# Performance work log

Hardware: AMD Instinct MI355X
Metric: run time of the kernel (lower is better)

The kernel has to match this reference:

```python
import jax, jax.numpy as jnp
import numpy as np

BLOCK_SIZE = 256
EMB = 384
HEAD = 64
B = 256
T = 256

def setup_inputs() -> dict:
    key = jax.random.key(0)
    k1, k2, k3, k4 = jax.random.split(key, 4)
    x = jax.random.normal(k1, (B, T, EMB), dtype=jnp.float32)
    # torch Linear(no bias) default init ~ U(-1/sqrt(in), 1/sqrt(in)); use scaled normal
    s = 1.0 / np.sqrt(EMB)
    Wq = jax.random.normal(k2, (EMB, HEAD), dtype=jnp.float32) * s
    Wk = jax.random.normal(k3, (EMB, HEAD), dtype=jnp.float32) * s
    Wv = jax.random.normal(k4, (EMB, HEAD), dtype=jnp.float32) * s
    return {"x": x, "Wq": Wq, "Wk": Wk, "Wv": Wv}

def reference(x, Wq, Wk, Wv):
    Bb, Tt, C = x.shape
    q = jnp.einsum('btc,ch->bth', x, Wq)
    k = jnp.einsum('btc,ch->bth', x, Wk)
    v = jnp.einsum('btc,ch->bth', x, Wv)
    # NOTE: source scales by C**-0.5 where C = embedding dim (384), not head_size
    scores = jnp.einsum('bth,bsh->bts', q, k) * (C ** -0.5)  # [B,T,T]
    causal = jnp.tril(jnp.ones((Tt, Tt), dtype=bool))
    scores = jnp.where(causal, scores, -jnp.inf)
    weights = jax.nn.softmax(scores, axis=-1)
    # dropout is identity in eval mode (reference baseline)
    out = jnp.einsum('bts,bsh->bth', weights, v)
    return out
```

## Files before the change

### kernel.cpp

```cpp
#include <hip/hip_runtime.h>
#include <hip/hip_bf16.h>
#include <cstdint>
#include <cstddef>

#define B_DIM 256
#define T_DIM 256
#define EMB   384
#define HEAD  64

typedef __attribute__((ext_vector_type(8))) short bf16x8;
typedef __attribute__((ext_vector_type(4))) float f32x4;
typedef __attribute__((ext_vector_type(4))) unsigned int u32x4;

__device__ __forceinline__ unsigned short f2bf(float f) {
    union { float f; unsigned int u; } v; v.f = f;
    unsigned int r = v.u + 0x7fffu + ((v.u >> 16) & 1u);
    return (unsigned short)(r >> 16);
}

__device__ __forceinline__ unsigned int pkbf(float a, float b) {
#if __has_builtin(__builtin_amdgcn_cvt_pk_bf16_f32)
    typedef __attribute__((ext_vector_type(2))) __bf16 bf16x2_t;
    bf16x2_t r = __builtin_amdgcn_cvt_pk_bf16_f32(a, b);
    return *(unsigned int*)&r;
#else
    return (unsigned)f2bf(a) | ((unsigned)f2bf(b) << 16);
#endif
}

__global__ void wprep_kernel(const float* __restrict__ Wq, const float* __restrict__ Wk,
                             const float* __restrict__ Wv, unsigned short* __restrict__ Wb) {
    int g = blockIdx.x * blockDim.x + threadIdx.x;
    if (g >= 9216) return;
    int kkstep = g / 1536, rem = g - kkstep * 1536;
    int r = rem >> 3, cs = rem & 7, c = cs ^ (r & 7);
    const float* W = (r < 64) ? Wq : (r < 128) ? Wk : Wv;
    int h = r & 63;
    unsigned short tmp[8];
#pragma unroll
    for (int e = 0; e < 8; ++e) {
        int k = kkstep * 64 + c * 8 + e;
        tmp[e] = f2bf(W[k * HEAD + h]);
    }
    *(u32x4*)(Wb + (size_t)g * 8) = *(u32x4*)tmp;
}

__global__ __launch_bounds__(1024, 1) void fused_kernel(const float* __restrict__ x,
                                                        const unsigned short* __restrict__ Wb,
                                                        float* __restrict__ out) {
    __shared__ union SM {
        struct { unsigned short Xs[2][256][72]; unsigned short Ws[2][12288]; } p1;
        struct { unsigned short qs[256][72]; unsigned short ks[256][72];
                 unsigned short vT[64][264]; unsigned short Ps[16][16][72]; } p2;
    } sm;

    const int tid = threadIdx.x;
    const int w = tid >> 6, lane = tid & 63, qd = lane >> 4, l15 = lane & 15;
    const int wm = w >> 2, wn = w & 3;
    const int b = blockIdx.x;
    const float* xb = x + (size_t)b * T_DIM * EMB;
    const int xrow = tid >> 2, xj = tid & 3;

#define WGLDS(KSTEP, BUF) do { \
    _Pragma("unroll") \
    for (int s = 0; s < 2; ++s) { \
        int idx = s * 1024 + w * 64; \
        if (idx < 1536) { \
            const unsigned short* gp = Wb + (size_t)((KSTEP) * 1536 + idx + lane) * 8; \
            unsigned short* lp = &sm.p1.Ws[BUF][idx * 8]; \
            __builtin_amdgcn_global_load_lds( \
                (const __attribute__((address_space(1))) unsigned int*)gp, \
                (__attribute__((address_space(3))) unsigned int*)lp, 16, 0, 0); \
        } \
    } \
} while (0)

#define XLOAD(KK) do { \
    _Pragma("unroll") \
    for (int i = 0; i < 4; ++i) \
        xr[i] = *(const float4*)(xb + (size_t)xrow * EMB + (KK) * 64 + (4 * xj + i) * 4); \
} while (0)

#define XWRITE(BUF) do { \
    _Pragma("unroll") \
    for (int i = 0; i < 4; ++i) \
        *(uint2*)&sm.p1.Xs[BUF][xrow][4 * (4 * xj + i)] = \
            make_uint2(pkbf(xr[i].x, xr[i].y), pkbf(xr[i].z, xr[i].w)); \
} while (0)

    float4 xr[4];
    WGLDS(0, 0);
    XLOAD(0);
    XWRITE(0);

    f32x4 acc[4][3];
#pragma unroll
    for (int mt = 0; mt < 4; ++mt)
#pragma unroll
        for (int nt = 0; nt < 3; ++nt) acc[mt][nt] = (f32x4){0.f, 0.f, 0.f, 0.f};

#pragma unroll
    for (int kk = 0; kk < 6; ++kk) {
        __syncthreads();
        if (kk < 5) {
            WGLDS(kk + 1, (kk + 1) & 1);
            XLOAD(kk + 1);
        }
#pragma unroll
        for (int kb = 0; kb < 2; ++kb) {
            bf16x8 a[4], bb[3];
#pragma unroll
            for (int mt = 0; mt < 4; ++mt)
                a[mt] = *(const bf16x8*)&sm.p1.Xs[kk & 1][64 * wm + 16 * mt + l15][32 * kb + 8 * qd];
#pragma unroll
            for (int nt = 0; nt < 3; ++nt) {
                int n = 48 * wn + 16 * nt + l15;
                bb[nt] = *(const bf16x8*)&sm.p1.Ws[kk & 1][n * 64 + (((4 * kb + qd) ^ (n & 7)) << 3)];
            }
#pragma unroll
            for (int mt = 0; mt < 4; ++mt)
#pragma unroll
                for (int nt = 0; nt < 3; ++nt)
                    acc[mt][nt] = __builtin_amdgcn_mfma_f32_16x16x32_bf16(a[mt], bb[nt], acc[mt][nt], 0, 0, 0);
        }
        if (kk < 5) XWRITE((kk + 1) & 1);
    }
    __syncthreads();

#pragma unroll
    for (int nt = 0; nt < 3; ++nt) {
        int n = 48 * wn + 16 * nt + l15;
        int arr = n >> 6, hh = n & 63;
        if (arr == 2) {
#pragma unroll
            for (int mt = 0; mt < 4; ++mt) {
                int tok0 = 64 * wm + 16 * mt + 4 * qd;
                *(uint2*)&sm.p2.vT[hh][tok0] = make_uint2(
                    pkbf(acc[mt][nt][0], acc[mt][nt][1]),
                    pkbf(acc[mt][nt][2], acc[mt][nt][3]));
            }
        } else {
#pragma unroll
            for (int mt = 0; mt < 4; ++mt)
#pragma unroll
                for (int reg = 0; reg < 4; ++reg) {
                    int tok = 64 * wm + 16 * mt + 4 * qd + reg;
                    unsigned short val = f2bf(acc[mt][nt][reg]);
                    if (arr == 0) sm.p2.qs[tok][hh] = val;
                    else          sm.p2.ks[tok][hh] = val;
                }
        }
    }
    __syncthreads();

    const int slot = w >> 2, sid = w & 3;
    const int t = (slot < 2) ? (2 * sid + slot) : (15 - 2 * sid - (slot & 1));

    bf16x8 aq[2];
#pragma unroll
    for (int kbi = 0; kbi < 2; ++kbi)
        aq[kbi] = *(const bf16x8*)&sm.p2.qs[16 * t + l15][32 * kbi + 8 * qd];

    f32x4 O[4];
    float l[4];
#pragma unroll
    for (int dn = 0; dn < 4; ++dn) O[dn] = (f32x4){0.f, 0.f, 0.f, 0.f};
#pragma unroll
    for (int reg = 0; reg < 4; ++reg) l[reg] = 0.f;

    const float cExp = 1.4426950408889634f / 19.595917942265423f;

    for (int jc = 0; jc <= (t >> 2); ++jc) {
        const int ntmax = min(3, t - 4 * jc);
        f32x4 S[4];
#pragma unroll
        for (int nt = 0; nt < 4; ++nt) {
            if (nt <= ntmax) {
                bf16x8 b0 = *(const bf16x8*)&sm.p2.ks[64 * jc + 16 * nt + l15][8 * qd];
                bf16x8 b1 = *(const bf16x8*)&sm.p2.ks[64 * jc + 16 * nt + l15][32 + 8 * qd];
                f32x4 s = __builtin_amdgcn_mfma_f32_16x16x32_bf16(aq[0], b0, (f32x4){0.f,0.f,0.f,0.f}, 0, 0, 0);
                s = __builtin_amdgcn_mfma_f32_16x16x32_bf16(aq[1], b1, s, 0, 0, 0);
                S[nt] = s;
            }
        }
#pragma unroll
        for (int nt = 0; nt < 4; ++nt) {
#pragma unroll
            for (int reg = 0; reg < 4; ++reg) {
                float p = 0.0f;
                if (nt <= ntmax) {
                    p = exp2f(S[nt][reg] * cExp);
                    if (4 * jc + nt == t && (l15 > 4 * qd + reg)) p = 0.0f;
                }
                l[reg] += p;
                sm.p2.Ps[w][4 * qd + reg][16 * nt + l15] = f2bf(p);
            }
        }
        bf16x8 ap0 = *(const bf16x8*)&sm.p2.Ps[w][l15][8 * qd];
        bf16x8 ap1 = *(const bf16x8*)&sm.p2.Ps[w][l15][32 + 8 * qd];
#pragma unroll
        for (int dn = 0; dn < 4; ++dn) {
            bf16x8 bv0 = *(const bf16x8*)&sm.p2.vT[16 * dn + l15][64 * jc + 8 * qd];
            bf16x8 bv1 = *(const bf16x8*)&sm.p2.vT[16 * dn + l15][64 * jc + 32 + 8 * qd];
            O[dn] = __builtin_amdgcn_mfma_f32_16x16x32_bf16(ap0, bv0, O[dn], 0, 0, 0);
            O[dn] = __builtin_amdgcn_mfma_f32_16x16x32_bf16(ap1, bv1, O[dn], 0, 0, 0);
        }
    }

#pragma unroll
    for (int reg = 0; reg < 4; ++reg) {
        float s = l[reg];
        s += __shfl_xor(s, 1);
        s += __shfl_xor(s, 2);
        s += __shfl_xor(s, 4);
        s += __shfl_xor(s, 8);
        float inv = 1.0f / s;
        int row = 16 * t + 4 * qd + reg;
        float* dst = out + ((size_t)b * T_DIM + row) * HEAD;
#pragma unroll
        for (int dn = 0; dn < 4; ++dn)
            dst[16 * dn + l15] = O[dn][reg] * inv;
    }
}

extern "C" void kernel_launch(void* const* d_in, const int* in_sizes, int n_in,
                              void* d_out, int out_size, void* d_ws, size_t ws_size,
                              hipStream_t stream) {
    const float* x  = (const float*)d_in[0];
    const float* Wq = (const float*)d_in[1];
    const float* Wk = (const float*)d_in[2];
    const float* Wv = (const float*)d_in[3];
    float* out = (float*)d_out;

    unsigned short* Wb = (unsigned short*)d_ws;

    wprep_kernel<<<36, 256, 0, stream>>>(Wq, Wk, Wv, Wb);
    fused_kernel<<<B_DIM, 1024, 0, stream>>>(x, Wb, out);
}
```

Before: 173.0 us.

## Warp-specialize projection GEMM into producer and consumer waves

The QKV projection phase now splits waves: 4 producer waves issue all global loads of x and W into LDS for the next stage, while 12 consumer waves run the MFMA projection with a 4x4 tile per wave (one of Q/K/V per wave column). This aims to overlap global memory latency with tensor math and drop load work from the compute waves. In exchange it removes a quarter of the waves from MFMA work, so each compute wave does more, and producer waves hold more registers.

```diff
diff --git a/kernel.cpp b/kernel.cpp
--- a/kernel.cpp
+++ b/kernel.cpp
@@ -56,99 +56,111 @@
 
     const int tid = threadIdx.x;
     const int w = tid >> 6, lane = tid & 63, qd = lane >> 4, l15 = lane & 15;
-    const int wm = w >> 2, wn = w & 3;
     const int b = blockIdx.x;
     const float* xb = x + (size_t)b * T_DIM * EMB;
-    const int xrow = tid >> 2, xj = tid & 3;
-
-#define WGLDS(KSTEP, BUF) do { \
+
+    const bool prod = (w >= 12);
+    const int wm = w & 3, wn2 = w >> 2;
+    const int pw = w - 12;
+    const int pt = tid & 255;
+    const int prow4 = pt >> 2, pj = pt & 3;
+
+#define PWGLDS(KSTEP, BUF) do { \
     _Pragma("unroll") \
-    for (int s = 0; s < 2; ++s) { \
-        int idx = s * 1024 + w * 64; \
-        if (idx < 1536) { \
-            const unsigned short* gp = Wb + (size_t)((KSTEP) * 1536 + idx + lane) * 8; \
-            unsigned short* lp = &sm.p1.Ws[BUF][idx * 8]; \
-            __builtin_amdgcn_global_load_lds( \
-                (const __attribute__((address_space(1))) unsigned int*)gp, \
-                (__attribute__((address_space(3))) unsigned int*)lp, 16, 0, 0); \
-        } \
+    for (int s = 0; s < 6; ++s) { \
+        int idx = s * 256 + pw * 64; \
+        const unsigned short* gp = Wb + (size_t)((KSTEP) * 1536 + idx + lane) * 8; \
+        unsigned short* lp = &sm.p1.Ws[BUF][idx * 8]; \
+        __builtin_amdgcn_global_load_lds( \
+            (const __attribute__((address_space(1))) unsigned int*)gp, \
+            (__attribute__((address_space(3))) unsigned int*)lp, 16, 0, 0); \
     } \
 } while (0)
 
-#define XLOAD(KK) do { \
+#define PXLOAD(KK) do { \
     _Pragma("unroll") \
-    for (int i = 0; i < 4; ++i) \
-        xr[i] = *(const float4*)(xb + (size_t)xrow * EMB + (KK) * 64 + (4 * xj + i) * 4); \
+    for (int s = 0; s < 4; ++s) \
+        _Pragma("unroll") \
+        for (int i = 0; i < 4; ++i) \
+            pxr[s][i] = *(const float4*)(xb + (size_t)(64 * s + prow4) * EMB + (KK) * 64 + (4 * pj + i) * 4); \
 } while (0)
 
-#define XWRITE(BUF) do { \
+#define PXWRITE(BUF) do { \
     _Pragma("unroll") \
-    for (int i = 0; i < 4; ++i) \
-        *(uint2*)&sm.p1.Xs[BUF][xrow][4 * (4 * xj + i)] = \
-            make_uint2(pkbf(xr[i].x, xr[i].y), pkbf(xr[i].z, xr[i].w)); \
+    for (int s = 0; s < 4; ++s) \
+        _Pragma("unroll") \
+        for (int i = 0; i < 4; ++i) \
+            *(uint2*)&sm.p1.Xs[BUF][64 * s + prow4][4 * (4 * pj + i)] = \
+                make_uint2(pkbf(pxr[s][i].x, pxr[s][i].y), pkbf(pxr[s][i].z, pxr[s][i].w)); \
 } while (0)
 
-    float4 xr[4];
-    WGLDS(0, 0);
-    XLOAD(0);
-    XWRITE(0);
-
-    f32x4 acc[4][3];
+    float4 pxr[4][4];
+    if (prod) {
+        PWGLDS(0, 0);
+        PXLOAD(0);
+        PXWRITE(0);
+    }
+
+    f32x4 acc[4][4];
 #pragma unroll
     for (int mt = 0; mt < 4; ++mt)
 #pragma unroll
-        for (int nt = 0; nt < 3; ++nt) acc[mt][nt] = (f32x4){0.f, 0.f, 0.f, 0.f};
+        for (int nt = 0; nt < 4; ++nt) acc[mt][nt] = (f32x4){0.f, 0.f, 0.f, 0.f};
 
 #pragma unroll
     for (int kk = 0; kk < 6; ++kk) {
         __syncthreads();
-        if (kk < 5) {
-            WGLDS(kk + 1, (kk + 1) & 1);
-            XLOAD(kk + 1);
-        }
-#pragma unroll
-        for (int kb = 0; kb < 2; ++kb) {
-            bf16x8 a[4], bb[3];
-#pragma unroll
-            for (int mt = 0; mt < 4; ++mt)
-                a[mt] = *(const bf16x8*)&sm.p1.Xs[kk & 1][64 * wm + 16 * mt + l15][32 * kb + 8 * qd];
-#pragma unroll
-            for (int nt = 0; nt < 3; ++nt) {
-                int n = 48 * wn + 16 * nt + l15;
-                bb[nt] = *(const bf16x8*)&sm.p1.Ws[kk & 1][n * 64 + (((4 * kb + qd) ^ (n & 7)) << 3)];
-            }
-#pragma unroll
-            for (int mt = 0; mt < 4; ++mt)
-#pragma unroll
-                for (int nt = 0; nt < 3; ++nt)
-                    acc[mt][nt] = __builtin_amdgcn_mfma_f32_16x16x32_bf16(a[mt], bb[nt], acc[mt][nt], 0, 0, 0);
-        }
-        if (kk < 5) XWRITE((kk + 1) & 1);
+        if (prod) {
+            if (kk < 5) {
+                PWGLDS(kk + 1, (kk + 1) & 1);
+                PXLOAD(kk + 1);
+                PXWRITE((kk + 1) & 1);
+            }
+        } else {
+#pragma unroll
+            for (int kb = 0; kb < 2; ++kb) {
+                bf16x8 a[4], bb[4];
+#pragma unroll
+                for (int mt = 0; mt < 4; ++mt)
+                    a[mt] = *(const bf16x8*)&sm.p1.Xs[kk & 1][64 * wm + 16 * mt + l15][32 * kb + 8 * qd];
+#pragma unroll
+                for (int nt = 0; nt < 4; ++nt) {
+                    int n = 64 * wn2 + 16 * nt + l15;
+                    bb[nt] = *(const bf16x8*)&sm.p1.Ws[kk & 1][n * 64 + (((4 * kb + qd) ^ (n & 7)) << 3)];
+                }
+#pragma unroll
+                for (int mt = 0; mt < 4; ++mt)
+#pragma unroll
+                    for (int nt = 0; nt < 4; ++nt)
+                        acc[mt][nt] = __builtin_amdgcn_mfma_f32_16x16x32_bf16(a[mt], bb[nt], acc[mt][nt], 0, 0, 0);
+            }
+        }
     }
     __syncthreads();
 
-#pragma unroll
-    for (int nt = 0; nt < 3; ++nt) {
-        int n = 48 * wn + 16 * nt + l15;
-        int arr = n >> 6, hh = n & 63;
-        if (arr == 2) {
-#pragma unroll
-            for (int mt = 0; mt < 4; ++mt) {
-                int tok0 = 64 * wm + 16 * mt + 4 * qd;
-                *(uint2*)&sm.p2.vT[hh][tok0] = make_uint2(
-                    pkbf(acc[mt][nt][0], acc[mt][nt][1]),
-                    pkbf(acc[mt][nt][2], acc[mt][nt][3]));
-            }
-        } else {
-#pragma unroll
-            for (int mt = 0; mt < 4; ++mt)
-#pragma unroll
-                for (int reg = 0; reg < 4; ++reg) {
-                    int tok = 64 * wm + 16 * mt + 4 * qd + reg;
-                    unsigned short val = f2bf(acc[mt][nt][reg]);
-                    if (arr == 0) sm.p2.qs[tok][hh] = val;
-                    else          sm.p2.ks[tok][hh] = val;
+    if (!prod) {
+#pragma unroll
+        for (int nt = 0; nt < 4; ++nt) {
+            int hh = 16 * nt + l15;
+            if (wn2 == 2) {
+#pragma unroll
+                for (int mt = 0; mt < 4; ++mt) {
+                    int tok0 = 64 * wm + 16 * mt + 4 * qd;
+                    *(uint2*)&sm.p2.vT[hh][tok0] = make_uint2(
+                        pkbf(acc[mt][nt][0], acc[mt][nt][1]),
+                        pkbf(acc[mt][nt][2], acc[mt][nt][3]));
                 }
+            } else {
+#pragma unroll
+                for (int mt = 0; mt < 4; ++mt)
+#pragma unroll
+                    for (int reg = 0; reg < 4; ++reg) {
+                        int tok = 64 * wm + 16 * mt + 4 * qd + reg;
+                        unsigned short val = f2bf(acc[mt][nt][reg]);
+                        if (wn2 == 0) sm.p2.qs[tok][hh] = val;
+                        else          sm.p2.ks[tok][hh] = val;
+                    }
+            }
         }
     }
     __syncthreads();
```

After: 172.4 us. No clear change (-0.3%).

## Load projection operands directly from global memory, dropping LDS staging

Applied to the files above, without the earlier changes.

The QKV projection no longer stages x and the packed weights through double-buffered shared memory. Each wave now reads its x rows straight from global memory, converts them to bf16 in registers, and loads weight fragments directly from the workspace. This removes the union'd LDS buffers and the per-step barriers. In exchange, the four waves sharing the same rows each fetch x redundantly, there is no software prefetch, and the k-loop is left un-unrolled, so global load latency is more exposed.

```diff
diff --git a/kernel.cpp b/kernel.cpp
--- a/kernel.cpp
+++ b/kernel.cpp
@@ -48,10 +48,9 @@
 __global__ __launch_bounds__(1024, 1) void fused_kernel(const float* __restrict__ x,
                                                         const unsigned short* __restrict__ Wb,
                                                         float* __restrict__ out) {
-    __shared__ union SM {
-        struct { unsigned short Xs[2][256][72]; unsigned short Ws[2][12288]; } p1;
-        struct { unsigned short qs[256][72]; unsigned short ks[256][72];
-                 unsigned short vT[64][264]; unsigned short Ps[16][16][72]; } p2;
+    __shared__ struct {
+        unsigned short qs[256][72]; unsigned short ks[256][72];
+        unsigned short vT[64][264]; unsigned short Ps[16][16][72];
     } sm;
 
     const int tid = threadIdx.x;
@@ -59,39 +58,6 @@
     const int wm = w >> 2, wn = w & 3;
     const int b = blockIdx.x;
     const float* xb = x + (size_t)b * T_DIM * EMB;
-    const int xrow = tid >> 2, xj = tid & 3;
-
-#define WGLDS(KSTEP, BUF) do { \
-    _Pragma("unroll") \
-    for (int s = 0; s < 2; ++s) { \
-        int idx = s * 1024 + w * 64; \
-        if (idx < 1536) { \
-            const unsigned short* gp = Wb + (size_t)((KSTEP) * 1536 + idx + lane) * 8; \
-            unsigned short* lp = &sm.p1.Ws[BUF][idx * 8]; \
-            __builtin_amdgcn_global_load_lds( \
-                (const __attribute__((address_space(1))) unsigned int*)gp, \
-                (__attribute__((address_space(3))) unsigned int*)lp, 16, 0, 0); \
-        } \
-    } \
-} while (0)
-
-#define XLOAD(KK) do { \
-    _Pragma("unroll") \
-    for (int i = 0; i < 4; ++i) \
-        xr[i] = *(const float4*)(xb + (size_t)xrow * EMB + (KK) * 64 + (4 * xj + i) * 4); \
-} while (0)
-
-#define XWRITE(BUF) do { \
-    _Pragma("unroll") \
-    for (int i = 0; i < 4; ++i) \
-        *(uint2*)&sm.p1.Xs[BUF][xrow][4 * (4 * xj + i)] = \
-            make_uint2(pkbf(xr[i].x, xr[i].y), pkbf(xr[i].z, xr[i].w)); \
-} while (0)
-
-    float4 xr[4];
-    WGLDS(0, 0);
-    XLOAD(0);
-    XWRITE(0);
 
     f32x4 acc[4][3];
 #pragma unroll
@@ -99,23 +65,34 @@
 #pragma unroll
         for (int nt = 0; nt < 3; ++nt) acc[mt][nt] = (f32x4){0.f, 0.f, 0.f, 0.f};
 
-#pragma unroll
+#pragma unroll 1
     for (int kk = 0; kk < 6; ++kk) {
-        __syncthreads();
-        if (kk < 5) {
-            WGLDS(kk + 1, (kk + 1) & 1);
-            XLOAD(kk + 1);
-        }
 #pragma unroll
         for (int kb = 0; kb < 2; ++kb) {
-            bf16x8 a[4], bb[3];
-#pragma unroll
-            for (int mt = 0; mt < 4; ++mt)
-                a[mt] = *(const bf16x8*)&sm.p1.Xs[kk & 1][64 * wm + 16 * mt + l15][32 * kb + 8 * qd];
+            float4 xa[4][2];
+#pragma unroll
+            for (int mt = 0; mt < 4; ++mt) {
+                const float* p = xb + (size_t)(64 * wm + 16 * mt + l15) * EMB
+                                 + kk * 64 + kb * 32 + 8 * qd;
+                xa[mt][0] = *(const float4*)p;
+                xa[mt][1] = *(const float4*)(p + 4);
+            }
+            bf16x8 bb[3];
 #pragma unroll
             for (int nt = 0; nt < 3; ++nt) {
                 int n = 48 * wn + 16 * nt + l15;
-                bb[nt] = *(const bf16x8*)&sm.p1.Ws[kk & 1][n * 64 + (((4 * kb + qd) ^ (n & 7)) << 3)];
+                bb[nt] = *(const bf16x8*)(Wb + (size_t)(kk * 1536 + n * 8 +
+                                                        (((kb << 2) + qd) ^ (n & 7))) * 8);
+            }
+            bf16x8 a[4];
+#pragma unroll
+            for (int mt = 0; mt < 4; ++mt) {
+                union { unsigned int u[4]; bf16x8 v; } cv;
+                cv.u[0] = pkbf(xa[mt][0].x, xa[mt][0].y);
+                cv.u[1] = pkbf(xa[mt][0].z, xa[mt][0].w);
+                cv.u[2] = pkbf(xa[mt][1].x, xa[mt][1].y);
+                cv.u[3] = pkbf(xa[mt][1].z, xa[mt][1].w);
+                a[mt] = cv.v;
             }
 #pragma unroll
             for (int mt = 0; mt < 4; ++mt)
@@ -123,9 +100,7 @@
                 for (int nt = 0; nt < 3; ++nt)
                     acc[mt][nt] = __builtin_amdgcn_mfma_f32_16x16x32_bf16(a[mt], bb[nt], acc[mt][nt], 0, 0, 0);
         }
-        if (kk < 5) XWRITE((kk + 1) & 1);
-    }
-    __syncthreads();
+    }
 
 #pragma unroll
     for (int nt = 0; nt < 3; ++nt) {
@@ -135,7 +110,7 @@
 #pragma unroll
             for (int mt = 0; mt < 4; ++mt) {
                 int tok0 = 64 * wm + 16 * mt + 4 * qd;
-                *(uint2*)&sm.p2.vT[hh][tok0] = make_uint2(
+                *(uint2*)&sm.vT[hh][tok0] = make_uint2(
                     pkbf(acc[mt][nt][0], acc[mt][nt][1]),
                     pkbf(acc[mt][nt][2], acc[mt][nt][3]));
             }
@@ -146,8 +121,8 @@
                 for (int reg = 0; reg < 4; ++reg) {
                     int tok = 64 * wm + 16 * mt + 4 * qd + reg;
                     unsigned short val = f2bf(acc[mt][nt][reg]);
-                    if (arr == 0) sm.p2.qs[tok][hh] = val;
-                    else          sm.p2.ks[tok][hh] = val;
+                    if (arr == 0) sm.qs[tok][hh] = val;
+                    else          sm.ks[tok][hh] = val;
                 }
         }
     }
@@ -159,7 +134,7 @@
     bf16x8 aq[2];
 #pragma unroll
     for (int kbi = 0; kbi < 2; ++kbi)
-        aq[kbi] = *(const bf16x8*)&sm.p2.qs[16 * t + l15][32 * kbi + 8 * qd];
+        aq[kbi] = *(const bf16x8*)&sm.qs[16 * t + l15][32 * kbi + 8 * qd];
 
     f32x4 O[4];
     float l[4];
@@ -176,8 +151,8 @@
 #pragma unroll
         for (int nt = 0; nt < 4; ++nt) {
             if (nt <= ntmax) {
-                bf16x8 b0 = *(const bf16x8*)&sm.p2.ks[64 * jc + 16 * nt + l15][8 * qd];
-                bf16x8 b1 = *(const bf16x8*)&sm.p2.ks[64 * jc + 16 * nt + l15][32 + 8 * qd];
+                bf16x8 b0 = *(const bf16x8*)&sm.ks[64 * jc + 16 * nt + l15][8 * qd];
+                bf16x8 b1 = *(const bf16x8*)&sm.ks[64 * jc + 16 * nt + l15][32 + 8 * qd];
                 f32x4 s = __builtin_amdgcn_mfma_f32_16x16x32_bf16(aq[0], b0, (f32x4){0.f,0.f,0.f,0.f}, 0, 0, 0);
                 s = __builtin_amdgcn_mfma_f32_16x16x32_bf16(aq[1], b1, s, 0, 0, 0);
                 S[nt] = s;
@@ -193,15 +168,15 @@
                     if (4 * jc + nt == t && (l15 > 4 * qd + reg)) p = 0.0f;
                 }
                 l[reg] += p;
-                sm.p2.Ps[w][4 * qd + reg][16 * nt + l15] = f2bf(p);
-            }
-        }
-        bf16x8 ap0 = *(const bf16x8*)&sm.p2.Ps[w][l15][8 * qd];
-        bf16x8 ap1 = *(const bf16x8*)&sm.p2.Ps[w][l15][32 + 8 * qd];
+                sm.Ps[w][4 * qd + reg][16 * nt + l15] = f2bf(p);
+            }
+        }
+        bf16x8 ap0 = *(const bf16x8*)&sm.Ps[w][l15][8 * qd];
+        bf16x8 ap1 = *(const bf16x8*)&sm.Ps[w][l15][32 + 8 * qd];
 #pragma unroll
         for (int dn = 0; dn < 4; ++dn) {
-            bf16x8 bv0 = *(const bf16x8*)&sm.p2.vT[16 * dn + l15][64 * jc + 8 * qd];
-            bf16x8 bv1 = *(const bf16x8*)&sm.p2.vT[16 * dn + l15][64 * jc + 32 + 8 * qd];
+            bf16x8 bv0 = *(const bf16x8*)&sm.vT[16 * dn + l15][64 * jc + 8 * qd];
+            bf16x8 bv1 = *(const bf16x8*)&sm.vT[16 * dn + l15][64 * jc + 32 + 8 * qd];
             O[dn] = __builtin_amdgcn_mfma_f32_16x16x32_bf16(ap0, bv0, O[dn], 0, 0, 0);
             O[dn] = __builtin_amdgcn_mfma_f32_16x16x32_bf16(ap1, bv1, O[dn], 0, 0, 0);
         }
```

Measured after the change: 190.7 us. +10.2%, slower.
